# Kernel optimization log

Hardware: AMD Instinct MI355X
Metric: run time of the kernel (lower is better)

The kernel has to match this reference:

```python
import jax, jax.numpy as jnp
import numpy as np

H = 256      # hidden_size (hardcoded by view([-1,1,256]) in the torch source)
V = 50257    # output_size / vocab
L = 50       # max_length


def gru_cell(x, h, w_ih, w_hh, b_ih, b_hh):
    """PyTorch GRUCell semantics. x, h: [H]; w_*: [3H, H]; b_*: [3H]."""
    gi = w_ih @ x + b_ih
    gh = w_hh @ h + b_hh
    gi_r, gi_z, gi_n = jnp.split(gi, 3)
    gh_r, gh_z, gh_n = jnp.split(gh, 3)
    r = jax.nn.sigmoid(gi_r + gh_r)
    z = jax.nn.sigmoid(gi_z + gh_z)
    n = jnp.tanh(gi_n + r * gh_n)
    return (1.0 - z) * n + z * h


def setup_inputs() -> dict:
    key = jax.random.key(0)
    ks = jax.random.split(key, 24)
    p = lambda k, shape: (0.02 * jax.random.normal(k, shape)).astype(jnp.float32)
    d = {}
    d["token"] = jax.random.randint(ks[0], (1,), 0, V)
    d["hidden"] = jax.random.normal(ks[1], (1, 1, H), dtype=jnp.float32)
    d["encoder_outputs"] = jax.random.normal(ks[2], (L, H), dtype=jnp.float32)
    d["emb"] = p(ks[3], (V, H))
    d["attn_W"] = p(ks[4], (L, 2 * H)); d["attn_b"] = jnp.zeros((L,), jnp.float32)
    d["comb_W"] = p(ks[5], (H, 2 * H)); d["comb_b"] = jnp.zeros((H,), jnp.float32)
    # bidirectional GRU: forward (f) and reverse (b) direction weights
    d["w_ih_f"] = p(ks[6], (3 * H, H)); d["w_hh_f"] = p(ks[7], (3 * H, H))
    d["b_ih_f"] = jnp.zeros((3 * H,), jnp.float32); d["b_hh_f"] = jnp.zeros((3 * H,), jnp.float32)
    d["w_ih_b"] = p(ks[8], (3 * H, H)); d["w_hh_b"] = p(ks[9], (3 * H, H))
    d["b_ih_b"] = jnp.zeros((3 * H,), jnp.float32); d["b_hh_b"] = jnp.zeros((3 * H,), jnp.float32)
    # second (unidirectional) GRU
    d["w_ih_g"] = p(ks[10], (3 * H, H)); d["w_hh_g"] = p(ks[11], (3 * H, H))
    d["b_ih_g"] = jnp.zeros((3 * H,), jnp.float32); d["b_hh_g"] = jnp.zeros((3 * H,), jnp.float32)
    d["out_W"] = p(ks[12], (V, H)); d["out_b"] = jnp.zeros((V,), jnp.float32)
    return d


def reference(token, hidden, encoder_outputs, emb, attn_W, attn_b, comb_W, comb_b,
              w_ih_f, w_hh_f, b_ih_f, b_hh_f, w_ih_b, w_hh_b, b_ih_b, b_hh_b,
              w_ih_g, w_hh_g, b_ih_g, b_hh_g, out_W, out_b):
    # dropout is treated as identity (eval mode)
    e = emb[token[0]]                       # [H] embedded token
    h0 = hidden[0, 0]                       # [H]
    # attention weights over encoder positions
    aw = jax.nn.softmax(jax.nn.relu(attn_W @ jnp.concatenate([e, h0]) + attn_b))  # [L]
    applied = aw @ encoder_outputs          # [H]
    x = jax.nn.relu(comb_W @ jnp.concatenate([e, applied]) + comb_b)              # [H]
    # bidirectional GRU, seq_len=1: both directions see the same step, init hidden = h0
    hf = gru_cell(x, h0, w_ih_f, w_hh_f, b_ih_f, b_hh_f)
    hb = gru_cell(x, h0, w_ih_b, w_hh_b, b_ih_b, b_hh_b)
    hm = 0.5 * (hf + hb)                    # torch.mean(bihidden, dim=0)
    # bioutput (1,1,512) viewed as (2,1,256) -> second GRU runs 2 steps
    h1 = gru_cell(hf, hm, w_ih_g, w_hh_g, b_ih_g, b_hh_g)
    h2 = gru_cell(hb, h1, w_ih_g, w_hh_g, b_ih_g, b_hh_g)
    logp = jax.nn.log_softmax(out_W @ h1 + out_b)  # output[0] = first timestep = h1
    return (logp[None, :], h2[None, None, :], aw[None, :])
```

## Files before the change

### kernel.cpp

```cpp
#include <hip/hip_runtime.h>
#include <math.h>

#define H 256
#define L 50
#define V 50257

__device__ __forceinline__ float dot4(float4 a, float4 b) {
    return a.x * b.x + a.y * b.y + a.z * b.z + a.w * b.w;
}

__device__ __forceinline__ float wave_reduce_sum(float v) {
#pragma unroll
    for (int m = 32; m >= 1; m >>= 1) v += __shfl_xor(v, m, 64);
    return v;
}

__device__ __forceinline__ float wave_reduce_max(float v) {
#pragma unroll
    for (int m = 32; m >= 1; m >>= 1) v = fmaxf(v, __shfl_xor(v, m, 64));
    return v;
}

__device__ __forceinline__ float sigmoidf(float x) { return 1.0f / (1.0f + __expf(-x)); }

__global__ __launch_bounds__(256) void k_attn(
    const int* __restrict__ token, const float* __restrict__ hidden,
    const float* __restrict__ enc, const float* __restrict__ emb,
    const float* __restrict__ attn_W, const float* __restrict__ attn_b,
    float* __restrict__ ws_cat, float* __restrict__ out_aw)
{
    __shared__ float s_vec[2 * H];
    __shared__ float s_scores[L];
    __shared__ float s_aw[L];
    int t = threadIdx.x;
    int tok = token[0];
    s_vec[t] = emb[(size_t)tok * H + t];
    s_vec[H + t] = hidden[t];
    __syncthreads();

    int wid = t >> 6, lane = t & 63;
    for (int l = wid; l < L; l += 4) {
        float acc = 0.f;
#pragma unroll
        for (int c = 0; c < 8; ++c)
            acc += attn_W[l * 2 * H + c * 64 + lane] * s_vec[c * 64 + lane];
        acc = wave_reduce_sum(acc);
        if (lane == 0) s_scores[l] = fmaxf(acc + attn_b[l], 0.f);
    }
    __syncthreads();

    if (t < 64) {
        float v = (t < L) ? s_scores[t] : -INFINITY;
        float m = wave_reduce_max(v);
        float e = (t < L) ? __expf(v - m) : 0.f;
        float s = wave_reduce_sum(e);
        float aw = e / s;
        if (t < L) { s_aw[t] = aw; out_aw[t] = aw; }
    }
    __syncthreads();

    float acc = 0.f;
    for (int l = 0; l < L; ++l) acc += s_aw[l] * enc[l * H + t];
    ws_cat[t] = s_vec[t];
    ws_cat[H + t] = acc;
}

__global__ __launch_bounds__(256) void k_comb(
    const float* __restrict__ comb_W, const float* __restrict__ comb_b,
    const float* __restrict__ ws_cat, float* __restrict__ ws_x)
{
    int t = threadIdx.x, wid = t >> 6, lane = t & 63;
    int row = blockIdx.x * 4 + wid;
    const float4* W4 = (const float4*)(comb_W + (size_t)row * 2 * H);
    const float4* c4 = (const float4*)ws_cat;
    float acc = dot4(W4[lane], c4[lane]) + dot4(W4[lane + 64], c4[lane + 64]);
    acc = wave_reduce_sum(acc);
    if (lane == 0) ws_x[row] = fmaxf(acc + comb_b[row], 0.f);
}

__global__ __launch_bounds__(256) void k_gru_fb(
    const float* __restrict__ ws_x, const float* __restrict__ hidden,
    const float* __restrict__ w_ih_f, const float* __restrict__ w_hh_f,
    const float* __restrict__ b_ih_f, const float* __restrict__ b_hh_f,
    const float* __restrict__ w_ih_b, const float* __restrict__ w_hh_b,
    const float* __restrict__ b_ih_b, const float* __restrict__ b_hh_b,
    float* __restrict__ ws_hf, float* __restrict__ ws_hb)
{
    int t = threadIdx.x, wid = t >> 6, lane = t & 63;
    int g = blockIdx.x * 4 + wid;
    int dir = g >> 8;
    int j = g & 255;
    const float* w_ih = dir ? w_ih_b : w_ih_f;
    const float* w_hh = dir ? w_hh_b : w_hh_f;
    const float* b_ih = dir ? b_ih_b : b_ih_f;
    const float* b_hh = dir ? b_hh_b : b_hh_f;
    float* outp = dir ? ws_hb : ws_hf;

    const float4* x4 = (const float4*)ws_x;
    const float4* h4 = (const float4*)hidden;
    float4 xv = x4[lane];
    float4 hv = h4[lane];
    float gi[3], gh[3];
#pragma unroll
    for (int k = 0; k < 3; ++k) {
        int row = k * H + j;
        const float4* wi4 = (const float4*)(w_ih + (size_t)row * H);
        const float4* wh4 = (const float4*)(w_hh + (size_t)row * H);
        gi[k] = wave_reduce_sum(dot4(wi4[lane], xv)) + b_ih[row];
        gh[k] = wave_reduce_sum(dot4(wh4[lane], hv)) + b_hh[row];
    }
    if (lane == 0) {
        float r = sigmoidf(gi[0] + gh[0]);
        float z = sigmoidf(gi[1] + gh[1]);
        float n = tanhf(gi[2] + r * gh[2]);
        outp[j] = (1.f - z) * n + z * hidden[j];
    }
}

__global__ __launch_bounds__(256) void k_gru(
    const float* __restrict__ xvec, const float* __restrict__ ha,
    const float* __restrict__ hb,
    const float* __restrict__ w_ih, const float* __restrict__ w_hh,
    const float* __restrict__ b_ih, const float* __restrict__ b_hh,
    float* __restrict__ outp)
{
    int t = threadIdx.x, wid = t >> 6, lane = t & 63;
    int j = blockIdx.x * 4 + wid;
    const float4* x4 = (const float4*)xvec;
    const float4* a4 = (const float4*)ha;
    float4 xv = x4[lane];
    float4 hv = a4[lane];
    float hj;
    if (hb) {
        const float4* b4 = (const float4*)hb;
        float4 bv = b4[lane];
        hv.x = 0.5f * (hv.x + bv.x);
        hv.y = 0.5f * (hv.y + bv.y);
        hv.z = 0.5f * (hv.z + bv.z);
        hv.w = 0.5f * (hv.w + bv.w);
        hj = 0.5f * (ha[j] + hb[j]);
    } else {
        hj = ha[j];
    }
    float gi[3], gh[3];
#pragma unroll
    for (int k = 0; k < 3; ++k) {
        int row = k * H + j;
        const float4* wi4 = (const float4*)(w_ih + (size_t)row * H);
        const float4* wh4 = (const float4*)(w_hh + (size_t)row * H);
        gi[k] = wave_reduce_sum(dot4(wi4[lane], xv)) + b_ih[row];
        gh[k] = wave_reduce_sum(dot4(wh4[lane], hv)) + b_hh[row];
    }
    if (lane == 0) {
        float r = sigmoidf(gi[0] + gh[0]);
        float z = sigmoidf(gi[1] + gh[1]);
        float n = tanhf(gi[2] + r * gh[2]);
        outp[j] = (1.f - z) * n + z * hj;
    }
}

__global__ __launch_bounds__(256) void k_logits(
    const float* __restrict__ out_W, const float* __restrict__ out_b,
    const float* __restrict__ h1, float* __restrict__ logits)
{
    int t = threadIdx.x, wid = t >> 6, lane = t & 63;
    int wave = blockIdx.x * 4 + wid;
    int nw = gridDim.x * 4;
    const float4* h4 = (const float4*)h1;
    float4 hv = h4[lane];
    for (int v = wave; v < V; v += nw) {
        const float4* W4 = (const float4*)(out_W + (size_t)v * H);
        float acc = wave_reduce_sum(dot4(W4[lane], hv));
        if (lane == 0) logits[v] = acc + out_b[v];
    }
}

__global__ __launch_bounds__(1024) void k_lse(
    const float* __restrict__ logits, float* __restrict__ ws_lse)
{
    __shared__ float red_m[16];
    __shared__ float red_s[16];
    int t = threadIdx.x, wid = t >> 6, lane = t & 63;
    float m = -INFINITY;
    for (int i = t; i < V; i += 1024) m = fmaxf(m, logits[i]);
    m = wave_reduce_max(m);
    if (lane == 0) red_m[wid] = m;
    __syncthreads();
    if (t == 0) {
        float v = red_m[0];
        for (int k = 1; k < 16; ++k) v = fmaxf(v, red_m[k]);
        red_m[0] = v;
    }
    __syncthreads();
    float gmax = red_m[0];
    float s = 0.f;
    for (int i = t; i < V; i += 1024) s += __expf(logits[i] - gmax);
    s = wave_reduce_sum(s);
    if (lane == 0) red_s[wid] = s;
    __syncthreads();
    if (t == 0) {
        float tot = 0.f;
        for (int k = 0; k < 16; ++k) tot += red_s[k];
        ws_lse[0] = gmax + logf(tot);
    }
}

__global__ __launch_bounds__(256) void k_sub(
    float* __restrict__ logits, const float* __restrict__ ws_lse)
{
    int i = blockIdx.x * blockDim.x + threadIdx.x;
    if (i < V) logits[i] -= ws_lse[0];
}

extern "C" void kernel_launch(void* const* d_in, const int* in_sizes, int n_in,
                              void* d_out, int out_size, void* d_ws, size_t ws_size,
                              hipStream_t stream)
{
    const int*   token  = (const int*)d_in[0];
    const float* hidden = (const float*)d_in[1];
    const float* enc    = (const float*)d_in[2];
    const float* emb    = (const float*)d_in[3];
    const float* attn_W = (const float*)d_in[4];
    const float* attn_b = (const float*)d_in[5];
    const float* comb_W = (const float*)d_in[6];
    const float* comb_b = (const float*)d_in[7];
    const float* w_ih_f = (const float*)d_in[8];
    const float* w_hh_f = (const float*)d_in[9];
    const float* b_ih_f = (const float*)d_in[10];
    const float* b_hh_f = (const float*)d_in[11];
    const float* w_ih_b = (const float*)d_in[12];
    const float* w_hh_b = (const float*)d_in[13];
    const float* b_ih_b = (const float*)d_in[14];
    const float* b_hh_b = (const float*)d_in[15];
    const float* w_ih_g = (const float*)d_in[16];
    const float* w_hh_g = (const float*)d_in[17];
    const float* b_ih_g = (const float*)d_in[18];
    const float* b_hh_g = (const float*)d_in[19];
    const float* out_W  = (const float*)d_in[20];
    const float* out_b  = (const float*)d_in[21];

    float* out = (float*)d_out;
    float* ws  = (float*)d_ws;
    float* ws_cat = ws;
    float* ws_x   = ws + 512;
    float* ws_hf  = ws + 768;
    float* ws_hb  = ws + 1024;
    float* ws_h1  = ws + 1280;
    float* ws_lse = ws + 1536;

    k_attn<<<1, 256, 0, stream>>>(token, hidden, enc, emb, attn_W, attn_b,
                                  ws_cat, out + V + H);
    k_comb<<<64, 256, 0, stream>>>(comb_W, comb_b, ws_cat, ws_x);
    k_gru_fb<<<128, 256, 0, stream>>>(ws_x, hidden,
                                      w_ih_f, w_hh_f, b_ih_f, b_hh_f,
                                      w_ih_b, w_hh_b, b_ih_b, b_hh_b,
                                      ws_hf, ws_hb);
    k_gru<<<64, 256, 0, stream>>>(ws_hf, ws_hf, ws_hb,
                                  w_ih_g, w_hh_g, b_ih_g, b_hh_g, ws_h1);
    k_gru<<<64, 256, 0, stream>>>(ws_hb, ws_h1, nullptr,
                                  w_ih_g, w_hh_g, b_ih_g, b_hh_g, out + V);
    k_logits<<<3142, 256, 0, stream>>>(out_W, out_b, ws_h1, out);
    k_lse<<<1, 1024, 0, stream>>>(out, ws_lse);
    k_sub<<<197, 256, 0, stream>>>(out, ws_lse);
}
```

Baseline: 202.2 us.

## Fuse all decoder stages into one cooperative kernel with online log-softmax

```diff
diff --git a/kernel.cpp b/kernel.cpp
--- a/kernel.cpp
+++ b/kernel.cpp
@@ -1,9 +1,16 @@
 #include <hip/hip_runtime.h>
+#include <hip/hip_cooperative_groups.h>
 #include <math.h>
+
+namespace cg = cooperative_groups;
 
 #define H 256
 #define L 50
 #define V 50257
+#define NBLK 512
+#define LOGIT_BLKS 448
+#define LOGIT_WAVES (LOGIT_BLKS * 4)
+#define ROWS_PER_WAVE 29
 
 __device__ __forceinline__ float dot4(float4 a, float4 b) {
     return a.x * b.x + a.y * b.y + a.z * b.z + a.w * b.w;
@@ -23,83 +30,12 @@
 
 __device__ __forceinline__ float sigmoidf(float x) { return 1.0f / (1.0f + __expf(-x)); }
 
-__global__ __launch_bounds__(256) void k_attn(
-    const int* __restrict__ token, const float* __restrict__ hidden,
-    const float* __restrict__ enc, const float* __restrict__ emb,
-    const float* __restrict__ attn_W, const float* __restrict__ attn_b,
-    float* __restrict__ ws_cat, float* __restrict__ out_aw)
+__device__ __forceinline__ void gru_wave(
+    int j, int lane, float4 xv, float4 hv, float hj,
+    const float* __restrict__ w_ih, const float* __restrict__ w_hh,
+    const float* __restrict__ b_ih, const float* __restrict__ b_hh,
+    float* __restrict__ outp)
 {
-    __shared__ float s_vec[2 * H];
-    __shared__ float s_scores[L];
-    __shared__ float s_aw[L];
-    int t = threadIdx.x;
-    int tok = token[0];
-    s_vec[t] = emb[(size_t)tok * H + t];
-    s_vec[H + t] = hidden[t];
-    __syncthreads();
-
-    int wid = t >> 6, lane = t & 63;
-    for (int l = wid; l < L; l += 4) {
-        float acc = 0.f;
-#pragma unroll
-        for (int c = 0; c < 8; ++c)
-            acc += attn_W[l * 2 * H + c * 64 + lane] * s_vec[c * 64 + lane];
-        acc = wave_reduce_sum(acc);
-        if (lane == 0) s_scores[l] = fmaxf(acc + attn_b[l], 0.f);
-    }
-    __syncthreads();
-
-    if (t < 64) {
-        float v = (t < L) ? s_scores[t] : -INFINITY;
-        float m = wave_reduce_max(v);
-        float e = (t < L) ? __expf(v - m) : 0.f;
-        float s = wave_reduce_sum(e);
-        float aw = e / s;
-        if (t < L) { s_aw[t] = aw; out_aw[t] = aw; }
-    }
-    __syncthreads();
-
-    float acc = 0.f;
-    for (int l = 0; l < L; ++l) acc += s_aw[l] * enc[l * H + t];
-    ws_cat[t] = s_vec[t];
-    ws_cat[H + t] = acc;
-}
-
-__global__ __launch_bounds__(256) void k_comb(
-    const float* __restrict__ comb_W, const float* __restrict__ comb_b,
-    const float* __restrict__ ws_cat, float* __restrict__ ws_x)
-{
-    int t = threadIdx.x, wid = t >> 6, lane = t & 63;
-    int row = blockIdx.x * 4 + wid;
-    const float4* W4 = (const float4*)(comb_W + (size_t)row * 2 * H);
-    const float4* c4 = (const float4*)ws_cat;
-    float acc = dot4(W4[lane], c4[lane]) + dot4(W4[lane + 64], c4[lane + 64]);
-    acc = wave_reduce_sum(acc);
-    if (lane == 0) ws_x[row] = fmaxf(acc + comb_b[row], 0.f);
-}
-
-__global__ __launch_bounds__(256) void k_gru_fb(
-    const float* __restrict__ ws_x, const float* __restrict__ hidden,
-    const float* __restrict__ w_ih_f, const float* __restrict__ w_hh_f,
-    const float* __restrict__ b_ih_f, const float* __restrict__ b_hh_f,
-    const float* __restrict__ w_ih_b, const float* __restrict__ w_hh_b,
-    const float* __restrict__ b_ih_b, const float* __restrict__ b_hh_b,
-    float* __restrict__ ws_hf, float* __restrict__ ws_hb)
-{
-    int t = threadIdx.x, wid = t >> 6, lane = t & 63;
-    int g = blockIdx.x * 4 + wid;
-    int dir = g >> 8;
-    int j = g & 255;
-    const float* w_ih = dir ? w_ih_b : w_ih_f;
-    const float* w_hh = dir ? w_hh_b : w_hh_f;
-    const float* b_ih = dir ? b_ih_b : b_ih_f;
-    const float* b_hh = dir ? b_hh_b : b_hh_f;
-    float* outp = dir ? ws_hb : ws_hf;
-
-    const float4* x4 = (const float4*)ws_x;
-    const float4* h4 = (const float4*)hidden;
-    float4 xv = x4[lane];
-    float4 hv = h4[lane];
     float gi[3], gh[3];
 #pragma unroll
     for (int k = 0; k < 3; ++k) {
@@ -113,103 +49,196 @@
         float r = sigmoidf(gi[0] + gh[0]);
         float z = sigmoidf(gi[1] + gh[1]);
         float n = tanhf(gi[2] + r * gh[2]);
-        outp[j] = (1.f - z) * n + z * hidden[j];
-    }
-}
-
-__global__ __launch_bounds__(256) void k_gru(
-    const float* __restrict__ xvec, const float* __restrict__ ha,
-    const float* __restrict__ hb,
-    const float* __restrict__ w_ih, const float* __restrict__ w_hh,
-    const float* __restrict__ b_ih, const float* __restrict__ b_hh,
-    float* __restrict__ outp)
+        outp[j] = (1.f - z) * n + z * hj;
+    }
+}
+
+__global__ __launch_bounds__(256, 2) void fused_decoder(
+    const int* __restrict__ token, const float* __restrict__ hidden,
+    const float* __restrict__ enc, const float* __restrict__ emb,
+    const float* __restrict__ attn_W, const float* __restrict__ attn_b,
+    const float* __restrict__ comb_W, const float* __restrict__ comb_b,
+    const float* __restrict__ w_ih_f, const float* __restrict__ w_hh_f,
+    const float* __restrict__ b_ih_f, const float* __restrict__ b_hh_f,
+    const float* __restrict__ w_ih_b, const float* __restrict__ w_hh_b,
+    const float* __restrict__ b_ih_b, const float* __restrict__ b_hh_b,
+    const float* __restrict__ w_ih_g, const float* __restrict__ w_hh_g,
+    const float* __restrict__ b_ih_g, const float* __restrict__ b_hh_g,
+    const float* __restrict__ out_W, const float* __restrict__ out_b,
+    float* __restrict__ out, float* __restrict__ ws)
 {
-    int t = threadIdx.x, wid = t >> 6, lane = t & 63;
-    int j = blockIdx.x * 4 + wid;
-    const float4* x4 = (const float4*)xvec;
-    const float4* a4 = (const float4*)ha;
-    float4 xv = x4[lane];
-    float4 hv = a4[lane];
-    float hj;
-    if (hb) {
-        const float4* b4 = (const float4*)hb;
-        float4 bv = b4[lane];
-        hv.x = 0.5f * (hv.x + bv.x);
-        hv.y = 0.5f * (hv.y + bv.y);
-        hv.z = 0.5f * (hv.z + bv.z);
-        hv.w = 0.5f * (hv.w + bv.w);
-        hj = 0.5f * (ha[j] + hb[j]);
+    cg::grid_group grid = cg::this_grid();
+
+    __shared__ float s_vec[2 * H];
+    __shared__ float s_scores[L];
+    __shared__ float s_aw[L];
+    __shared__ float s_m[4], s_s[4];
+    __shared__ float s_bcast;
+
+    const int b = blockIdx.x, t = threadIdx.x;
+    const int wid = t >> 6, lane = t & 63;
+
+    float* ws_cat = ws;
+    float* ws_x   = ws + 512;
+    float* ws_hf  = ws + 768;
+    float* ws_hb  = ws + 1024;
+    float* ws_h1  = ws + 1280;
+    float* ws_m   = ws + 1536;
+    float* ws_s   = ws + 2048;
+
+    if (b == 0) {
+        int tok = token[0];
+        s_vec[t] = emb[(size_t)tok * H + t];
+        s_vec[H + t] = hidden[t];
+        __syncthreads();
+
+        for (int l = wid; l < L; l += 4) {
+            float acc = 0.f;
+#pragma unroll
+            for (int c = 0; c < 8; ++c)
+                acc += attn_W[l * 2 * H + c * 64 + lane] * s_vec[c * 64 + lane];
+            acc = wave_reduce_sum(acc);
+            if (lane == 0) s_scores[l] = fmaxf(acc + attn_b[l], 0.f);
+        }
+        __syncthreads();
+
+        if (t < 64) {
+            float v = (t < L) ? s_scores[t] : -INFINITY;
+            float m = wave_reduce_max(v);
+            float e = (t < L) ? __expf(v - m) : 0.f;
+            float s = wave_reduce_sum(e);
+            float aw = e / s;
+            if (t < L) { s_aw[t] = aw; out[V + H + t] = aw; }
+        }
+        __syncthreads();
+
+        float acc = 0.f;
+        for (int l = 0; l < L; ++l) acc += s_aw[l] * enc[l * H + t];
+        ws_cat[t] = s_vec[t];
+        ws_cat[H + t] = acc;
+    }
+    grid.sync();
+
+    if (b < 64) {
+        int row = b * 4 + wid;
+        const float4* W4 = (const float4*)(comb_W + (size_t)row * 2 * H);
+        const float4* c4 = (const float4*)ws_cat;
+        float acc = dot4(W4[lane], c4[lane]) + dot4(W4[lane + 64], c4[lane + 64]);
+        acc = wave_reduce_sum(acc);
+        if (lane == 0) ws_x[row] = fmaxf(acc + comb_b[row], 0.f);
+    }
+    grid.sync();
+
+    if (b < 128) {
+        int g = b * 4 + wid;
+        int dir = g >> 8;
+        int j = g & 255;
+        const float4* x4 = (const float4*)ws_x;
+        const float4* h4 = (const float4*)hidden;
+        gru_wave(j, lane, x4[lane], h4[lane], hidden[j],
+                 dir ? w_ih_b : w_ih_f, dir ? w_hh_b : w_hh_f,
+                 dir ? b_ih_b : b_ih_f, dir ? b_hh_b : b_hh_f,
+                 dir ? ws_hb : ws_hf);
+    }
+    grid.sync();
+
+    if (b < 64) {
+        int j = b * 4 + wid;
+        const float4* x4 = (const float4*)ws_hf;
+        const float4* a4 = (const float4*)ws_hf;
+        const float4* b4 = (const float4*)ws_hb;
+        float4 av = a4[lane], bv = b4[lane];
+        float4 hv = make_float4(0.5f * (av.x + bv.x), 0.5f * (av.y + bv.y),
+                                0.5f * (av.z + bv.z), 0.5f * (av.w + bv.w));
+        float hj = 0.5f * (ws_hf[j] + ws_hb[j]);
+        gru_wave(j, lane, x4[lane], hv, hj,
+                 w_ih_g, w_hh_g, b_ih_g, b_hh_g, ws_h1);
+    }
+    grid.sync();
+
+    if (b >= LOGIT_BLKS) {
+        int j = (b - LOGIT_BLKS) * 4 + wid;
+        const float4* x4 = (const float4*)ws_hb;
+        const float4* h4 = (const float4*)ws_h1;
+        gru_wave(j, lane, x4[lane], h4[lane], ws_h1[j],
+                 w_ih_g, w_hh_g, b_ih_g, b_hh_g, out + V);
+        if (t == 0) { ws_m[b] = -INFINITY; ws_s[b] = 0.f; }
     } else {
-        hj = ha[j];
-    }
-    float gi[3], gh[3];
-#pragma unroll
-    for (int k = 0; k < 3; ++k) {
-        int row = k * H + j;
-        const float4* wi4 = (const float4*)(w_ih + (size_t)row * H);
-        const float4* wh4 = (const float4*)(w_hh + (size_t)row * H);
-        gi[k] = wave_reduce_sum(dot4(wi4[lane], xv)) + b_ih[row];
-        gh[k] = wave_reduce_sum(dot4(wh4[lane], hv)) + b_hh[row];
-    }
-    if (lane == 0) {
-        float r = sigmoidf(gi[0] + gh[0]);
-        float z = sigmoidf(gi[1] + gh[1]);
-        float n = tanhf(gi[2] + r * gh[2]);
-        outp[j] = (1.f - z) * n + z * hj;
-    }
-}
-
-__global__ __launch_bounds__(256) void k_logits(
-    const float* __restrict__ out_W, const float* __restrict__ out_b,
-    const float* __restrict__ h1, float* __restrict__ logits)
-{
-    int t = threadIdx.x, wid = t >> 6, lane = t & 63;
-    int wave = blockIdx.x * 4 + wid;
-    int nw = gridDim.x * 4;
-    const float4* h4 = (const float4*)h1;
-    float4 hv = h4[lane];
-    for (int v = wave; v < V; v += nw) {
-        const float4* W4 = (const float4*)(out_W + (size_t)v * H);
-        float acc = wave_reduce_sum(dot4(W4[lane], hv));
-        if (lane == 0) logits[v] = acc + out_b[v];
-    }
-}
-
-__global__ __launch_bounds__(1024) void k_lse(
-    const float* __restrict__ logits, float* __restrict__ ws_lse)
-{
-    __shared__ float red_m[16];
-    __shared__ float red_s[16];
-    int t = threadIdx.x, wid = t >> 6, lane = t & 63;
-    float m = -INFINITY;
-    for (int i = t; i < V; i += 1024) m = fmaxf(m, logits[i]);
-    m = wave_reduce_max(m);
-    if (lane == 0) red_m[wid] = m;
-    __syncthreads();
-    if (t == 0) {
-        float v = red_m[0];
-        for (int k = 1; k < 16; ++k) v = fmaxf(v, red_m[k]);
-        red_m[0] = v;
-    }
-    __syncthreads();
-    float gmax = red_m[0];
-    float s = 0.f;
-    for (int i = t; i < V; i += 1024) s += __expf(logits[i] - gmax);
-    s = wave_reduce_sum(s);
-    if (lane == 0) red_s[wid] = s;
-    __syncthreads();
-    if (t == 0) {
-        float tot = 0.f;
-        for (int k = 0; k < 16; ++k) tot += red_s[k];
-        ws_lse[0] = gmax + logf(tot);
-    }
-}
-
-__global__ __launch_bounds__(256) void k_sub(
-    float* __restrict__ logits, const float* __restrict__ ws_lse)
-{
-    int i = blockIdx.x * blockDim.x + threadIdx.x;
-    if (i < V) logits[i] -= ws_lse[0];
+        const int wave = b * 4 + wid;
+        const float4* h4 = (const float4*)ws_h1;
+        float4 hv = h4[lane];
+        int start = wave * ROWS_PER_WAVE;
+        int end = min(start + ROWS_PER_WAVE, V);
+        float m = -INFINITY, s = 0.f;
+        for (int v = start; v < end; v += 2) {
+            const float4* W0 = (const float4*)(out_W + (size_t)v * H);
+            float4 a0 = W0[lane];
+            bool has2 = (v + 1 < end);
+            float4 a1 = has2 ? ((const float4*)(out_W + (size_t)(v + 1) * H))[lane]
+                             : make_float4(0.f, 0.f, 0.f, 0.f);
+            float x0 = wave_reduce_sum(dot4(a0, hv)) + out_b[v];
+            float x1 = wave_reduce_sum(dot4(a1, hv));
+            if (lane == 0) out[v] = x0;
+            float mn = fmaxf(m, x0);
+            s = s * __expf(m - mn) + __expf(x0 - mn);
+            m = mn;
+            if (has2) {
+                x1 += out_b[v + 1];
+                if (lane == 0) out[v + 1] = x1;
+                mn = fmaxf(m, x1);
+                s = s * __expf(m - mn) + __expf(x1 - mn);
+                m = mn;
+            }
+        }
+        if (lane == 0) { s_m[wid] = m; s_s[wid] = s; }
+        __syncthreads();
+        if (t == 0) {
+            float M = s_m[0], S = s_s[0];
+#pragma unroll
+            for (int k = 1; k < 4; ++k) {
+                float mk = s_m[k], sk = s_s[k];
+                float mn = fmaxf(M, mk);
+                S = (M > -INFINITY ? S * __expf(M - mn) : 0.f) +
+                    (mk > -INFINITY ? sk * __expf(mk - mn) : 0.f);
+                M = mn;
+            }
+            ws_m[b] = M; ws_s[b] = S;
+        }
+    }
+    grid.sync();
+
+    {
+        float m1 = ws_m[t], s1 = ws_s[t];
+        float m2 = ws_m[t + 256], s2 = ws_s[t + 256];
+        float M = fmaxf(m1, m2);
+        float s = s1 * __expf(m1 - M) + (m2 > -INFINITY ? s2 * __expf(m2 - M) : 0.f);
+        float m = M;
+#pragma unroll
+        for (int d = 32; d >= 1; d >>= 1) {
+            float om = __shfl_xor(m, d, 64);
+            float os = __shfl_xor(s, d, 64);
+            float mn = fmaxf(m, om);
+            s = s * __expf(m - mn) + os * __expf(om - mn);
+            m = mn;
+        }
+        if (lane == 0) { s_m[wid] = m; s_s[wid] = s; }
+        __syncthreads();
+        if (t == 0) {
+            float M2 = s_m[0], S2 = s_s[0];
+#pragma unroll
+            for (int k = 1; k < 4; ++k) {
+                float mk = s_m[k], sk = s_s[k];
+                float mn = fmaxf(M2, mk);
+                S2 = S2 * __expf(M2 - mn) + sk * __expf(mk - mn);
+                M2 = mn;
+            }
+            s_bcast = M2 + logf(S2);
+        }
+        __syncthreads();
+        float lse = s_bcast;
+        int i = b * 256 + t;
+        if (i < V) out[i] -= lse;
+    }
 }
 
 extern "C" void kernel_launch(void* const* d_in, const int* in_sizes, int n_in,
@@ -238,28 +267,17 @@
     const float* b_hh_g = (const float*)d_in[19];
     const float* out_W  = (const float*)d_in[20];
     const float* out_b  = (const float*)d_in[21];
-
     float* out = (float*)d_out;
     float* ws  = (float*)d_ws;
-    float* ws_cat = ws;
-    float* ws_x   = ws + 512;
-    float* ws_hf  = ws + 768;
-    float* ws_hb  = ws + 1024;
-    float* ws_h1  = ws + 1280;
-    float* ws_lse = ws + 1536;
-
-    k_attn<<<1, 256, 0, stream>>>(token, hidden, enc, emb, attn_W, attn_b,
-                                  ws_cat, out + V + H);
-    k_comb<<<64, 256, 0, stream>>>(comb_W, comb_b, ws_cat, ws_x);
-    k_gru_fb<<<128, 256, 0, stream>>>(ws_x, hidden,
-                                      w_ih_f, w_hh_f, b_ih_f, b_hh_f,
-                                      w_ih_b, w_hh_b, b_ih_b, b_hh_b,
-                                      ws_hf, ws_hb);
-    k_gru<<<64, 256, 0, stream>>>(ws_hf, ws_hf, ws_hb,
-                                  w_ih_g, w_hh_g, b_ih_g, b_hh_g, ws_h1);
-    k_gru<<<64, 256, 0, stream>>>(ws_hb, ws_h1, nullptr,
-                                  w_ih_g, w_hh_g, b_ih_g, b_hh_g, out + V);
-    k_logits<<<3142, 256, 0, stream>>>(out_W, out_b, ws_h1, out);
-    k_lse<<<1, 1024, 0, stream>>>(out, ws_lse);
-    k_sub<<<197, 256, 0, stream>>>(out, ws_lse);
-}
+
+    void* args[] = {
+        (void*)&token, (void*)&hidden, (void*)&enc, (void*)&emb,
+        (void*)&attn_W, (void*)&attn_b, (void*)&comb_W, (void*)&comb_b,
+        (void*)&w_ih_f, (void*)&w_hh_f, (void*)&b_ih_f, (void*)&b_hh_f,
+        (void*)&w_ih_b, (void*)&w_hh_b, (void*)&b_ih_b, (void*)&b_hh_b,
+        (void*)&w_ih_g, (void*)&w_hh_g, (void*)&b_ih_g, (void*)&b_hh_g,
+        (void*)&out_W, (void*)&out_b, (void*)&out, (void*)&ws,
+    };
+    hipLaunchCooperativeKernel((const void*)fused_decoder,
+                               dim3(NBLK), dim3(256), args, 0, stream);
+}
```

New measurement: 496.9 us. +145.7%, slower.

## Fuse online log-softmax into logits kernel and parallelize attention scoring

Applied to the files above, without the earlier changes.

```diff
diff --git a/kernel.cpp b/kernel.cpp
--- a/kernel.cpp
+++ b/kernel.cpp
@@ -4,6 +4,7 @@
 #define H 256
 #define L 50
 #define V 50257
+#define LOGIT_BLKS 786
 
 __device__ __forceinline__ float dot4(float4 a, float4 b) {
     return a.x * b.x + a.y * b.y + a.z * b.z + a.w * b.w;
@@ -23,56 +24,93 @@
 
 __device__ __forceinline__ float sigmoidf(float x) { return 1.0f / (1.0f + __expf(-x)); }
 
-__global__ __launch_bounds__(256) void k_attn(
+__device__ __forceinline__ void ms_push(float& m, float& s, float x) {
+    float mn = fmaxf(m, x);
+    s = s * __expf(m - mn) + __expf(x - mn);
+    m = mn;
+}
+__device__ __forceinline__ void ms_merge(float& m, float& s, float om, float os) {
+    float M = fmaxf(m, om);
+    float a = (m == -INFINITY) ? 0.f : s * __expf(m - M);
+    float c = (om == -INFINITY) ? 0.f : os * __expf(om - M);
+    m = M; s = a + c;
+}
+
+__device__ __forceinline__ void gru_wave(
+    int j, int lane, float4 xv, float4 hv, float hj,
+    const float* __restrict__ w_ih, const float* __restrict__ w_hh,
+    const float* __restrict__ b_ih, const float* __restrict__ b_hh,
+    float* __restrict__ outp)
+{
+    float gi[3], gh[3];
+#pragma unroll
+    for (int k = 0; k < 3; ++k) {
+        int row = k * H + j;
+        const float4* wi4 = (const float4*)(w_ih + (size_t)row * H);
+        const float4* wh4 = (const float4*)(w_hh + (size_t)row * H);
+        gi[k] = wave_reduce_sum(dot4(wi4[lane], xv)) + b_ih[row];
+        gh[k] = wave_reduce_sum(dot4(wh4[lane], hv)) + b_hh[row];
+    }
+    if (lane == 0) {
+        float r = sigmoidf(gi[0] + gh[0]);
+        float z = sigmoidf(gi[1] + gh[1]);
+        float n = tanhf(gi[2] + r * gh[2]);
+        outp[j] = (1.f - z) * n + z * hj;
+    }
+}
+
+__global__ __launch_bounds__(256) void k_scores(
     const int* __restrict__ token, const float* __restrict__ hidden,
-    const float* __restrict__ enc, const float* __restrict__ emb,
-    const float* __restrict__ attn_W, const float* __restrict__ attn_b,
-    float* __restrict__ ws_cat, float* __restrict__ out_aw)
+    const float* __restrict__ emb, const float* __restrict__ attn_W,
+    const float* __restrict__ attn_b, float* __restrict__ ws_scores)
 {
     __shared__ float s_vec[2 * H];
-    __shared__ float s_scores[L];
-    __shared__ float s_aw[L];
-    int t = threadIdx.x;
+    int t = threadIdx.x, wid = t >> 6, lane = t & 63;
     int tok = token[0];
     s_vec[t] = emb[(size_t)tok * H + t];
     s_vec[H + t] = hidden[t];
     __syncthreads();
-
-    int wid = t >> 6, lane = t & 63;
-    for (int l = wid; l < L; l += 4) {
+    int row = blockIdx.x * 4 + wid;
+    if (row < L) {
         float acc = 0.f;
 #pragma unroll
         for (int c = 0; c < 8; ++c)
-            acc += attn_W[l * 2 * H + c * 64 + lane] * s_vec[c * 64 + lane];
+            acc += attn_W[row * 2 * H + c * 64 + lane] * s_vec[c * 64 + lane];
         acc = wave_reduce_sum(acc);
-        if (lane == 0) s_scores[l] = fmaxf(acc + attn_b[l], 0.f);
-    }
-    __syncthreads();
-
+        if (lane == 0) ws_scores[row] = fmaxf(acc + attn_b[row], 0.f);
+    }
+}
+
+__global__ __launch_bounds__(256) void k_comb(
+    const int* __restrict__ token, const float* __restrict__ emb,
+    const float* __restrict__ enc, const float* __restrict__ comb_W,
+    const float* __restrict__ comb_b, const float* __restrict__ ws_scores,
+    float* __restrict__ ws_x, float* __restrict__ out_aw)
+{
+    __shared__ __align__(16) float s_cat[2 * H];
+    __shared__ float s_aw[64];
+    int t = threadIdx.x, wid = t >> 6, lane = t & 63;
+    int tok = token[0];
+    s_cat[t] = emb[(size_t)tok * H + t];
     if (t < 64) {
-        float v = (t < L) ? s_scores[t] : -INFINITY;
-        float m = wave_reduce_max(v);
-        float e = (t < L) ? __expf(v - m) : 0.f;
-        float s = wave_reduce_sum(e);
-        float aw = e / s;
-        if (t < L) { s_aw[t] = aw; out_aw[t] = aw; }
-    }
-    __syncthreads();
-
-    float acc = 0.f;
-    for (int l = 0; l < L; ++l) acc += s_aw[l] * enc[l * H + t];
-    ws_cat[t] = s_vec[t];
-    ws_cat[H + t] = acc;
-}
-
-__global__ __launch_bounds__(256) void k_comb(
-    const float* __restrict__ comb_W, const float* __restrict__ comb_b,
-    const float* __restrict__ ws_cat, float* __restrict__ ws_x)
-{
-    int t = threadIdx.x, wid = t >> 6, lane = t & 63;
+        float v = (t < L) ? ws_scores[t] : -INFINITY;
+        float mx = wave_reduce_max(v);
+        float e = (t < L) ? __expf(v - mx) : 0.f;
+        float ssum = wave_reduce_sum(e);
+        if (t < L) {
+            float aw = e / ssum;
+            s_aw[t] = aw;
+            if (blockIdx.x == 0) out_aw[t] = aw;
+        }
+    }
+    __syncthreads();
+    float app = 0.f;
+    for (int l = 0; l < L; ++l) app += s_aw[l] * enc[l * H + t];
+    s_cat[H + t] = app;
+    __syncthreads();
     int row = blockIdx.x * 4 + wid;
+    const float4* c4 = (const float4*)s_cat;
     const float4* W4 = (const float4*)(comb_W + (size_t)row * 2 * H);
-    const float4* c4 = (const float4*)ws_cat;
     float acc = dot4(W4[lane], c4[lane]) + dot4(W4[lane + 64], c4[lane + 64]);
     acc = wave_reduce_sum(acc);
     if (lane == 0) ws_x[row] = fmaxf(acc + comb_b[row], 0.f);
@@ -88,33 +126,12 @@
 {
     int t = threadIdx.x, wid = t >> 6, lane = t & 63;
     int g = blockIdx.x * 4 + wid;
-    int dir = g >> 8;
-    int j = g & 255;
-    const float* w_ih = dir ? w_ih_b : w_ih_f;
-    const float* w_hh = dir ? w_hh_b : w_hh_f;
-    const float* b_ih = dir ? b_ih_b : b_ih_f;
-    const float* b_hh = dir ? b_hh_b : b_hh_f;
-    float* outp = dir ? ws_hb : ws_hf;
-
-    const float4* x4 = (const float4*)ws_x;
-    const float4* h4 = (const float4*)hidden;
-    float4 xv = x4[lane];
-    float4 hv = h4[lane];
-    float gi[3], gh[3];
-#pragma unroll
-    for (int k = 0; k < 3; ++k) {
-        int row = k * H + j;
-        const float4* wi4 = (const float4*)(w_ih + (size_t)row * H);
-        const float4* wh4 = (const float4*)(w_hh + (size_t)row * H);
-        gi[k] = wave_reduce_sum(dot4(wi4[lane], xv)) + b_ih[row];
-        gh[k] = wave_reduce_sum(dot4(wh4[lane], hv)) + b_hh[row];
-    }
-    if (lane == 0) {
-        float r = sigmoidf(gi[0] + gh[0]);
-        float z = sigmoidf(gi[1] + gh[1]);
-        float n = tanhf(gi[2] + r * gh[2]);
-        outp[j] = (1.f - z) * n + z * hidden[j];
-    }
+    int dir = g >> 8, j = g & 255;
+    gru_wave(j, lane, ((const float4*)ws_x)[lane], ((const float4*)hidden)[lane],
+             hidden[j],
+             dir ? w_ih_b : w_ih_f, dir ? w_hh_b : w_hh_f,
+             dir ? b_ih_b : b_ih_f, dir ? b_hh_b : b_hh_f,
+             dir ? ws_hb : ws_hf);
 }
 
 __global__ __launch_bounds__(256) void k_gru(
@@ -126,90 +143,87 @@
 {
     int t = threadIdx.x, wid = t >> 6, lane = t & 63;
     int j = blockIdx.x * 4 + wid;
-    const float4* x4 = (const float4*)xvec;
-    const float4* a4 = (const float4*)ha;
-    float4 xv = x4[lane];
-    float4 hv = a4[lane];
+    float4 xv = ((const float4*)xvec)[lane];
+    float4 hv = ((const float4*)ha)[lane];
     float hj;
     if (hb) {
-        const float4* b4 = (const float4*)hb;
-        float4 bv = b4[lane];
-        hv.x = 0.5f * (hv.x + bv.x);
-        hv.y = 0.5f * (hv.y + bv.y);
-        hv.z = 0.5f * (hv.z + bv.z);
-        hv.w = 0.5f * (hv.w + bv.w);
+        float4 bv = ((const float4*)hb)[lane];
+        hv = make_float4(0.5f * (hv.x + bv.x), 0.5f * (hv.y + bv.y),
+                         0.5f * (hv.z + bv.z), 0.5f * (hv.w + bv.w));
         hj = 0.5f * (ha[j] + hb[j]);
     } else {
         hj = ha[j];
     }
-    float gi[3], gh[3];
-#pragma unroll
-    for (int k = 0; k < 3; ++k) {
-        int row = k * H + j;
-        const float4* wi4 = (const float4*)(w_ih + (size_t)row * H);
-        const float4* wh4 = (const float4*)(w_hh + (size_t)row * H);
-        gi[k] = wave_reduce_sum(dot4(wi4[lane], xv)) + b_ih[row];
-        gh[k] = wave_reduce_sum(dot4(wh4[lane], hv)) + b_hh[row];
-    }
-    if (lane == 0) {
-        float r = sigmoidf(gi[0] + gh[0]);
-        float z = sigmoidf(gi[1] + gh[1]);
-        float n = tanhf(gi[2] + r * gh[2]);
-        outp[j] = (1.f - z) * n + z * hj;
-    }
+    gru_wave(j, lane, xv, hv, hj, w_ih, w_hh, b_ih, b_hh, outp);
 }
 
 __global__ __launch_bounds__(256) void k_logits(
     const float* __restrict__ out_W, const float* __restrict__ out_b,
-    const float* __restrict__ h1, float* __restrict__ logits)
-{
-    int t = threadIdx.x, wid = t >> 6, lane = t & 63;
-    int wave = blockIdx.x * 4 + wid;
-    int nw = gridDim.x * 4;
-    const float4* h4 = (const float4*)h1;
-    float4 hv = h4[lane];
-    for (int v = wave; v < V; v += nw) {
-        const float4* W4 = (const float4*)(out_W + (size_t)v * H);
-        float acc = wave_reduce_sum(dot4(W4[lane], hv));
-        if (lane == 0) logits[v] = acc + out_b[v];
-    }
-}
-
-__global__ __launch_bounds__(1024) void k_lse(
-    const float* __restrict__ logits, float* __restrict__ ws_lse)
-{
-    __shared__ float red_m[16];
-    __shared__ float red_s[16];
-    int t = threadIdx.x, wid = t >> 6, lane = t & 63;
-    float m = -INFINITY;
-    for (int i = t; i < V; i += 1024) m = fmaxf(m, logits[i]);
-    m = wave_reduce_max(m);
-    if (lane == 0) red_m[wid] = m;
+    const float* __restrict__ h1, float* __restrict__ logits,
+    float* __restrict__ part_m, float* __restrict__ part_s)
+{
+    __shared__ float s_m4[4], s_s4[4];
+    int t = threadIdx.x, wid = t >> 6, lane = t & 63;
+    float4 hv = ((const float4*)h1)[lane];
+    int base = (blockIdx.x * 4 + wid) * 16;
+    float m = -INFINITY, s = 0.f;
+#pragma unroll 1
+    for (int k = 0; k < 16; k += 2) {
+        int v = base + k;
+        if (v >= V) break;
+        const float4* W0 = (const float4*)(out_W + (size_t)v * H);
+        float4 a0 = W0[lane];
+        bool has2 = (v + 1 < V);
+        float4 a1 = has2 ? ((const float4*)(out_W + (size_t)(v + 1) * H))[lane]
+                         : make_float4(0.f, 0.f, 0.f, 0.f);
+        float x0 = wave_reduce_sum(dot4(a0, hv)) + out_b[v];
+        float x1 = wave_reduce_sum(dot4(a1, hv));
+        if (lane == 0) logits[v] = x0;
+        ms_push(m, s, x0);
+        if (has2) {
+            x1 += out_b[v + 1];
+            if (lane == 0) logits[v + 1] = x1;
+            ms_push(m, s, x1);
+        }
+    }
+    if (lane == 0) { s_m4[wid] = m; s_s4[wid] = s; }
     __syncthreads();
     if (t == 0) {
-        float v = red_m[0];
-        for (int k = 1; k < 16; ++k) v = fmaxf(v, red_m[k]);
-        red_m[0] = v;
-    }
-    __syncthreads();
-    float gmax = red_m[0];
-    float s = 0.f;
-    for (int i = t; i < V; i += 1024) s += __expf(logits[i] - gmax);
-    s = wave_reduce_sum(s);
-    if (lane == 0) red_s[wid] = s;
+        float M = s_m4[0], S = s_s4[0];
+#pragma unroll
+        for (int q = 1; q < 4; ++q) ms_merge(M, S, s_m4[q], s_s4[q]);
+        part_m[blockIdx.x] = M; part_s[blockIdx.x] = S;
+    }
+}
+
+__global__ __launch_bounds__(256) void k_final(
+    const float* __restrict__ part_m, const float* __restrict__ part_s,
+    float* __restrict__ logits)
+{
+    __shared__ float s_m4[4], s_s4[4];
+    __shared__ float s_bcast;
+    int t = threadIdx.x, wid = t >> 6, lane = t & 63;
+    float m = -INFINITY, s = 0.f;
+    for (int idx = t; idx < LOGIT_BLKS; idx += 256)
+        ms_merge(m, s, part_m[idx], part_s[idx]);
+#pragma unroll
+    for (int d = 32; d >= 1; d >>= 1) {
+        float om = __shfl_xor(m, d, 64);
+        float os = __shfl_xor(s, d, 64);
+        ms_merge(m, s, om, os);
+    }
+    if (lane == 0) { s_m4[wid] = m; s_s4[wid] = s; }
     __syncthreads();
     if (t == 0) {
-        float tot = 0.f;
-        for (int k = 0; k < 16; ++k) tot += red_s[k];
-        ws_lse[0] = gmax + logf(tot);
-    }
-}
-
-__global__ __launch_bounds__(256) void k_sub(
-    float* __restrict__ logits, const float* __restrict__ ws_lse)
-{
-    int i = blockIdx.x * blockDim.x + threadIdx.x;
-    if (i < V) logits[i] -= ws_lse[0];
+        float M = s_m4[0], S = s_s4[0];
+#pragma unroll
+        for (int q = 1; q < 4; ++q) ms_merge(M, S, s_m4[q], s_s4[q]);
+        s_bcast = M + logf(S);
+    }
+    __syncthreads();
+    float lse = s_bcast;
+    int i = blockIdx.x * 256 + t;
+    if (i < V) logits[i] -= lse;
 }
 
 extern "C" void kernel_launch(void* const* d_in, const int* in_sizes, int n_in,
@@ -241,16 +255,17 @@
 
     float* out = (float*)d_out;
     float* ws  = (float*)d_ws;
-    float* ws_cat = ws;
-    float* ws_x   = ws + 512;
-    float* ws_hf  = ws + 768;
-    float* ws_hb  = ws + 1024;
-    float* ws_h1  = ws + 1280;
-    float* ws_lse = ws + 1536;
-
-    k_attn<<<1, 256, 0, stream>>>(token, hidden, enc, emb, attn_W, attn_b,
-                                  ws_cat, out + V + H);
-    k_comb<<<64, 256, 0, stream>>>(comb_W, comb_b, ws_cat, ws_x);
+    float* ws_scores = ws;
+    float* ws_x      = ws + 64;
+    float* ws_hf     = ws + 320;
+    float* ws_hb     = ws + 576;
+    float* ws_h1     = ws + 832;
+    float* part_m    = ws + 1088;
+    float* part_s    = ws + 1888;
+
+    k_scores<<<13, 256, 0, stream>>>(token, hidden, emb, attn_W, attn_b, ws_scores);
+    k_comb<<<64, 256, 0, stream>>>(token, emb, enc, comb_W, comb_b, ws_scores,
+                                   ws_x, out + V + H);
     k_gru_fb<<<128, 256, 0, stream>>>(ws_x, hidden,
                                       w_ih_f, w_hh_f, b_ih_f, b_hh_f,
                                       w_ih_b, w_hh_b, b_ih_b, b_hh_b,
@@ -259,7 +274,7 @@
                                   w_ih_g, w_hh_g, b_ih_g, b_hh_g, ws_h1);
     k_gru<<<64, 256, 0, stream>>>(ws_hb, ws_h1, nullptr,
                                   w_ih_g, w_hh_g, b_ih_g, b_hh_g, out + V);
-    k_logits<<<3142, 256, 0, stream>>>(out_W, out_b, ws_h1, out);
-    k_lse<<<1, 1024, 0, stream>>>(out, ws_lse);
-    k_sub<<<197, 256, 0, stream>>>(out, ws_lse);
-}
+    k_logits<<<LOGIT_BLKS, 256, 0, stream>>>(out_W, out_b, ws_h1, out,
+                                             part_m, part_s);
+    k_final<<<197, 256, 0, stream>>>(part_m, part_s, out);
+}
```

Measured after the change: 177.8 us. 12.1% less time.
